# Kernel optimization log

Measured on AMD Instinct MI355X. Metric: run time of the kernel, lower is better.

Reference implementation:

```python
import jax, jax.numpy as jnp
import numpy as np

IN, H, T = 1024, 2048, 2048

def setup_inputs() -> dict:
    key = jax.random.key(0)
    ks = jax.random.split(key, 10)
    x = jax.random.normal(ks[0], (1, T, IN), dtype=jnp.float32)
    # strictly increasing timestamps
    time = jnp.cumsum(jax.random.uniform(ks[1], (T,), dtype=jnp.float32))
    # xavier-ish scaled weights, uniform(0,1) biases as in init_weights
    W_ih = jax.random.normal(ks[2], (4 * H, IN), dtype=jnp.float32) * (1.0 / np.sqrt(IN))
    W_hh = jax.random.normal(ks[3], (4 * H, H), dtype=jnp.float32) * (1.0 / np.sqrt(H))
    b_ih = jax.random.uniform(ks[4], (4 * H,), dtype=jnp.float32)
    b_hh = jax.random.uniform(ks[5], (4 * H,), dtype=jnp.float32)
    decay_w = jax.random.normal(ks[6], (H,), dtype=jnp.float32)
    decay_b = jax.random.uniform(ks[7], (H,), dtype=jnp.float32)
    h0 = jax.random.normal(ks[8], (1, H), dtype=jnp.float32) * 0.1
    c0 = jax.random.normal(ks[9], (1, H), dtype=jnp.float32) * 0.1
    return {"x": x, "time": time, "W_ih": W_ih, "W_hh": W_hh, "b_ih": b_ih,
            "b_hh": b_hh, "decay_w": decay_w, "decay_b": decay_b, "h0": h0, "c0": c0}


def reference(x, time, W_ih, W_hh, b_ih, b_hh, decay_w, decay_b, h0, c0):
    Tn = x.shape[1]
    Hn = h0.shape[1]
    # dt[i] = time[i] - time[i-1], dt[0] = 0
    dt = jnp.concatenate([jnp.zeros((1,), x.dtype), time[1:] - time[:-1]])
    # step i (i>0) decays h with gamma(dt[i-1]); step 0 uses gamma = 1
    dt_prev = jnp.concatenate([jnp.zeros((1,), x.dtype), dt[:-1]])  # [T]
    gamma = jnp.exp(-jax.nn.relu(dt_prev[:, None] * decay_w[None, :] + decay_b[None, :]))  # [T,H]
    gamma = jnp.where((jnp.arange(Tn) > 0)[:, None], gamma, jnp.ones((), x.dtype))
    # precompute input contribution for all steps: [T, 4H]
    xg = x[0] @ W_ih.T + b_ih + b_hh

    def step(carry, inp):
        h, c = carry  # [H], [H]
        xg_t, gamma_t = inp
        h = h * gamma_t
        gates = xg_t + h @ W_hh.T  # [4H]
        i_, f_, g_, o_ = jnp.split(gates, 4)
        i_ = jax.nn.sigmoid(i_)
        f_ = jax.nn.sigmoid(f_)
        g_ = jnp.tanh(g_)
        o_ = jax.nn.sigmoid(o_)
        c = f_ * c + i_ * g_
        h = o_ * jnp.tanh(c)
        return (h, c), h

    (h_f, c_f), hs = jax.lax.scan(step, (h0[0], c0[0]), (xg, gamma))  # hs: [T,H]
    # dot-product attention pooling against final hidden state
    attn = hs @ h_f  # [T]
    w = jax.nn.softmax(attn)
    context = w @ hs  # [H]
    return context[None, :]  # [1, H]
```

## Files before the change

kernel.cpp:

```cpp
#include <hip/hip_runtime.h>
#include <hip/hip_bf16.h>

#define H 2048
#define T 2048
#define INPUT 1024
#define FOURH 8192
#define NBLK 256
#define RING 512

typedef __attribute__((ext_vector_type(8))) short bf16x8;
typedef __attribute__((ext_vector_type(4))) float f32x4_t;

__device__ __forceinline__ short f2bf(float f) {
  union { float f; unsigned u; } v; v.f = f;
  unsigned r = v.u + 0x7FFFu + ((v.u >> 16) & 1u);
  return (short)(r >> 16);
}

__global__ void prep_kernel(const float* __restrict__ x, const float* __restrict__ W_ih,
                            const float* __restrict__ time_, short* __restrict__ xb,
                            short* __restrict__ wb, float* __restrict__ dtp,
                            unsigned* __restrict__ flags) {
  size_t i = (size_t)blockIdx.x * blockDim.x + threadIdx.x;
  size_t stride = (size_t)gridDim.x * blockDim.x;
  if (i < (size_t)T * INPUT) xb[i] = f2bf(x[i]);
  for (size_t j = i; j < (size_t)FOURH * INPUT; j += stride) wb[j] = f2bf(W_ih[j]);
  if (i < T) dtp[i] = (i >= 2) ? (time_[i - 1] - time_[i - 2]) : 0.0f;
  if (i < NBLK) flags[i] = 0u;
}

__global__ void __launch_bounds__(256)
gemm_xg(const short* __restrict__ A, const short* __restrict__ B,
        const float* __restrict__ b_ih, const float* __restrict__ b_hh,
        float* __restrict__ xg) {
  int wave = threadIdx.x >> 6;
  int lane = threadIdx.x & 63;
  int m0 = blockIdx.y << 4;
  int n0 = (blockIdx.x << 6) + (wave << 4);
  int r16 = lane & 15, q = lane >> 4;
  const short* ap = A + (size_t)(m0 + r16) * INPUT + q * 8;
  const short* bp = B + (size_t)(n0 + r16) * INPUT + q * 8;
  f32x4_t acc = {0.f, 0.f, 0.f, 0.f};
#pragma unroll 4
  for (int k = 0; k < INPUT; k += 32) {
    bf16x8 av = *(const bf16x8*)(ap + k);
    bf16x8 bv = *(const bf16x8*)(bp + k);
    acc = __builtin_amdgcn_mfma_f32_16x16x32_bf16(av, bv, acc, 0, 0, 0);
  }
  int n = n0 + r16;
  float bias = b_ih[n] + b_hh[n];
#pragma unroll
  for (int r = 0; r < 4; ++r) {
    int m = m0 + q * 4 + r;
    xg[(size_t)m * FOURH + n] = acc[r] + bias;
  }
}

__device__ __forceinline__ void epoch_bar(unsigned* flags, unsigned e) {
  __syncthreads();
  if (threadIdx.x == 0)
    __hip_atomic_store(&flags[blockIdx.x], e, __ATOMIC_RELEASE, __HIP_MEMORY_SCOPE_AGENT);
  if (threadIdx.x < NBLK) {
    while (__hip_atomic_load(&flags[threadIdx.x], __ATOMIC_RELAXED,
                             __HIP_MEMORY_SCOPE_AGENT) < e) {
    }
  }
  __builtin_amdgcn_fence(__ATOMIC_ACQUIRE, "agent");
  __syncthreads();
}

__global__ void __launch_bounds__(512, 2)
lstm_rec(const float* __restrict__ xg, const float* __restrict__ W_hh,
         const float* __restrict__ decay_w, const float* __restrict__ decay_b,
         const float* __restrict__ h0, const float* __restrict__ c0,
         const float* __restrict__ dtp, float* __restrict__ hs,
         unsigned long long* ring, unsigned* flags) {
  const int wave = threadIdx.x >> 6;
  const int lane = threadIdx.x & 63;
  const int u = (blockIdx.x << 3) + wave;
  __shared__ float lh[H];

  float wreg[4][32];
#pragma unroll
  for (int g = 0; g < 4; ++g) {
    const float* wr = W_hh + (size_t)(g * H + u) * H + lane;
#pragma unroll
    for (int j = 0; j < 32; ++j) wreg[g][j] = wr[(size_t)j << 6];
  }
  const float dw = decay_w[u], db = decay_b[u];
  float c = c0[u];
  if (lane == 0) {
    union { float f; unsigned u; } hv; hv.f = h0[u];
    __hip_atomic_store(&ring[u], (1ull << 32) | hv.u, __ATOMIC_RELAXED,
                       __HIP_MEMORY_SCOPE_AGENT);
  }

  for (int t = 0; t < T; ++t) {
    if ((t & 255) == 0 && t) epoch_bar(flags, (unsigned)(t >> 8));

    float xi = 0.f, xf = 0.f, xgv = 0.f, xo = 0.f, dtn = 0.f;
    if (lane == 0) {
      const float* xr = xg + (size_t)t * FOURH;
      xi = xr[u]; xf = xr[H + u]; xgv = xr[2 * H + u]; xo = xr[3 * H + u];
      if (t + 1 < T) dtn = dtp[t + 1];
    }

    const unsigned want = (unsigned)t + 1u;
    unsigned long long* sp =
        ring + (((size_t)(t & (RING - 1)) << 11) | (unsigned)((wave << 8) + lane));
    unsigned long long w0, w1, w2, w3;
    for (;;) {
      w0 = __hip_atomic_load(sp,       __ATOMIC_RELAXED, __HIP_MEMORY_SCOPE_AGENT);
      w1 = __hip_atomic_load(sp + 64,  __ATOMIC_RELAXED, __HIP_MEMORY_SCOPE_AGENT);
      w2 = __hip_atomic_load(sp + 128, __ATOMIC_RELAXED, __HIP_MEMORY_SCOPE_AGENT);
      w3 = __hip_atomic_load(sp + 192, __ATOMIC_RELAXED, __HIP_MEMORY_SCOPE_AGENT);
      int bad = ((unsigned)(w0 >> 32) != want) | ((unsigned)(w1 >> 32) != want) |
                ((unsigned)(w2 >> 32) != want) | ((unsigned)(w3 >> 32) != want);
      if (!__any(bad)) break;
    }
    {
      float* lw = lh + (wave << 8) + lane;
      union { unsigned u; float f; } v;
      v.u = (unsigned)w0; lw[0]   = v.f;
      v.u = (unsigned)w1; lw[64]  = v.f;
      v.u = (unsigned)w2; lw[128] = v.f;
      v.u = (unsigned)w3; lw[192] = v.f;
    }
    __syncthreads();

    float a0 = 0.f, a1 = 0.f, a2 = 0.f, a3 = 0.f;
#pragma unroll
    for (int j = 0; j < 32; ++j) {
      float h = lh[(j << 6) + lane];
      a0 += wreg[0][j] * h;
      a1 += wreg[1][j] * h;
      a2 += wreg[2][j] * h;
      a3 += wreg[3][j] * h;
    }
#pragma unroll
    for (int s = 32; s >= 1; s >>= 1) {
      a0 += __shfl_xor(a0, s);
      a1 += __shfl_xor(a1, s);
      a2 += __shfl_xor(a2, s);
      a3 += __shfl_xor(a3, s);
    }
    if (lane == 0) {
      float iv = a0 + xi;
      float fv = a1 + xf;
      float gv = a2 + xgv;
      float ov = a3 + xo;
      iv = 1.f / (1.f + __expf(-iv));
      fv = 1.f / (1.f + __expf(-fv));
      gv = tanhf(gv);
      ov = 1.f / (1.f + __expf(-ov));
      c = fv * c + iv * gv;
      float h = ov * tanhf(c);
      hs[(size_t)t * H + u] = h;
      if (t + 1 < T) {
        float gam = __expf(-fmaxf(0.f, dtn * dw + db));
        union { float f; unsigned u; } hv; hv.f = h * gam;
        size_t slot = (size_t)((t + 1) & (RING - 1)) << 11;
        __hip_atomic_store(&ring[slot | (unsigned)u],
                           (((unsigned long long)(t + 2)) << 32) | hv.u,
                           __ATOMIC_RELAXED, __HIP_MEMORY_SCOPE_AGENT);
      }
    }
    __syncthreads();
  }
}

__global__ void attn_k(const float* __restrict__ hs, float* __restrict__ attn) {
  int t = blockIdx.x;
  const float* row = hs + (size_t)t * H;
  const float* hf = hs + (size_t)(T - 1) * H;
  float s = 0.f;
  for (int i = threadIdx.x; i < H; i += 256) s += row[i] * hf[i];
#pragma unroll
  for (int o = 32; o; o >>= 1) s += __shfl_down(s, o);
  __shared__ float wsum[4];
  if ((threadIdx.x & 63) == 0) wsum[threadIdx.x >> 6] = s;
  __syncthreads();
  if (threadIdx.x == 0) attn[t] = wsum[0] + wsum[1] + wsum[2] + wsum[3];
}

__global__ void softmax_k(float* __restrict__ a) {
  int tid = threadIdx.x;
  __shared__ float red[16];
  __shared__ float bcast;
  float m = -1e30f;
  for (int i = tid; i < T; i += 1024) m = fmaxf(m, a[i]);
#pragma unroll
  for (int o = 32; o; o >>= 1) m = fmaxf(m, __shfl_xor(m, o));
  if ((tid & 63) == 0) red[tid >> 6] = m;
  __syncthreads();
  if (tid == 0) {
    float mm = red[0];
    for (int i = 1; i < 16; ++i) mm = fmaxf(mm, red[i]);
    bcast = mm;
  }
  __syncthreads();
  float M = bcast, s = 0.f;
  for (int i = tid; i < T; i += 1024) { float e = __expf(a[i] - M); a[i] = e; s += e; }
#pragma unroll
  for (int o = 32; o; o >>= 1) s += __shfl_xor(s, o);
  if ((tid & 63) == 0) red[tid >> 6] = s;
  __syncthreads();
  if (tid == 0) {
    float ss = 0.f;
    for (int i = 0; i < 16; ++i) ss += red[i];
    bcast = 1.f / ss;
  }
  __syncthreads();
  float inv = bcast;
  for (int i = tid; i < T; i += 1024) a[i] *= inv;
}

__global__ void ctx_k(const float* __restrict__ hs, const float* __restrict__ w,
                      float* __restrict__ out) {
  int h = (blockIdx.x << 8) + threadIdx.x;
  int t0 = blockIdx.y << 6;
  float acc = 0.f;
  for (int t = t0; t < t0 + 64; ++t) acc += w[t] * hs[(size_t)t * H + h];
  atomicAdd(&out[h], acc);
}

extern "C" void kernel_launch(void* const* d_in, const int* in_sizes, int n_in,
                              void* d_out, int out_size, void* d_ws, size_t ws_size,
                              hipStream_t stream) {
  const float* x       = (const float*)d_in[0];
  const float* time_   = (const float*)d_in[1];
  const float* W_ih    = (const float*)d_in[2];
  const float* W_hh    = (const float*)d_in[3];
  const float* b_ih    = (const float*)d_in[4];
  const float* b_hh    = (const float*)d_in[5];
  const float* decay_w = (const float*)d_in[6];
  const float* decay_b = (const float*)d_in[7];
  const float* h0      = (const float*)d_in[8];
  const float* c0      = (const float*)d_in[9];

  char* ws = (char*)d_ws;
  float*    xg   = (float*)ws;
  float*    hs   = (float*)(ws + (64u << 20));
  short*    xb   = (short*)(ws + (80u << 20));
  short*    wb   = (short*)(ws + (84u << 20));
  unsigned long long* ring = (unsigned long long*)(ws + (100u << 20));
  float*    dtp  = (float*)(ws + (108u << 20));
  float*    attn = dtp + T;
  unsigned* flags = (unsigned*)(attn + T);

  prep_kernel<<<8192, 256, 0, stream>>>(x, W_ih, time_, xb, wb, dtp, flags);

  dim3 g1(FOURH / 64, T / 16);
  gemm_xg<<<g1, 256, 0, stream>>>(xb, wb, b_ih, b_hh, xg);

  {
    void* args[] = {&xg, (void*)&W_hh, (void*)&decay_w, (void*)&decay_b,
                    (void*)&h0, (void*)&c0, &dtp, &hs, &ring, &flags};
    (void)hipLaunchCooperativeKernel((void*)lstm_rec, dim3(NBLK), dim3(512), args, 0, stream);
  }

  attn_k<<<T, 256, 0, stream>>>(hs, attn);
  softmax_k<<<1, 1024, 0, stream>>>(attn);
  (void)hipMemsetAsync(d_out, 0, out_size * sizeof(float), stream);
  ctx_k<<<dim3(H / 256, T / 64), 256, 0, stream>>>(hs, attn, (float*)d_out);
}
```

Before: 6.799 ms.

## Vectorize recurrent LDS reads, precompute decay early, reorder GEMM grid

The recurrent kernel now loads W_hh into registers and reads the hidden state from LDS as 16-byte float4 vectors, with each lane owning four contiguous elements. This replaces 32 scalar LDS reads per step with 8 vector reads. The decay factor is computed before the ring spin-wait, off the critical path, and the ring store is issued before the hs store so other blocks see the new state sooner. The xg GEMM switches to a 1D grid that walks M fastest, changing block scheduling order and cache reuse of the weight tiles.

```diff
diff --git a/kernel.cpp b/kernel.cpp
--- a/kernel.cpp
+++ b/kernel.cpp
@@ -11,10 +11,10 @@
 typedef __attribute__((ext_vector_type(8))) short bf16x8;
 typedef __attribute__((ext_vector_type(4))) float f32x4_t;
 
-__device__ __forceinline__ short f2bf(float f) {
+__device__ __forceinline__ unsigned short f2bf(float f) {
   union { float f; unsigned u; } v; v.f = f;
   unsigned r = v.u + 0x7FFFu + ((v.u >> 16) & 1u);
-  return (short)(r >> 16);
+  return (unsigned short)(r >> 16);
 }
 
 __global__ void prep_kernel(const float* __restrict__ x, const float* __restrict__ W_ih,
@@ -23,8 +23,8 @@
                             unsigned* __restrict__ flags) {
   size_t i = (size_t)blockIdx.x * blockDim.x + threadIdx.x;
   size_t stride = (size_t)gridDim.x * blockDim.x;
-  if (i < (size_t)T * INPUT) xb[i] = f2bf(x[i]);
-  for (size_t j = i; j < (size_t)FOURH * INPUT; j += stride) wb[j] = f2bf(W_ih[j]);
+  if (i < (size_t)T * INPUT) xb[i] = (short)f2bf(x[i]);
+  for (size_t j = i; j < (size_t)FOURH * INPUT; j += stride) wb[j] = (short)f2bf(W_ih[j]);
   if (i < T) dtp[i] = (i >= 2) ? (time_[i - 1] - time_[i - 2]) : 0.0f;
   if (i < NBLK) flags[i] = 0u;
 }
@@ -35,8 +35,9 @@
         float* __restrict__ xg) {
   int wave = threadIdx.x >> 6;
   int lane = threadIdx.x & 63;
-  int m0 = blockIdx.y << 4;
-  int n0 = (blockIdx.x << 6) + (wave << 4);
+  int bid = blockIdx.x;
+  int m0 = (bid & 127) << 4;
+  int n0 = ((bid >> 7) << 6) + (wave << 4);
   int r16 = lane & 15, q = lane >> 4;
   const short* ap = A + (size_t)(m0 + r16) * INPUT + q * 8;
   const short* bp = B + (size_t)(n0 + r16) * INPUT + q * 8;
@@ -78,14 +79,15 @@
   const int wave = threadIdx.x >> 6;
   const int lane = threadIdx.x & 63;
   const int u = (blockIdx.x << 3) + wave;
-  __shared__ float lh[H];
+  __shared__ __align__(16) float lh[H];
 
   float wreg[4][32];
 #pragma unroll
   for (int g = 0; g < 4; ++g) {
-    const float* wr = W_hh + (size_t)(g * H + u) * H + lane;
-#pragma unroll
-    for (int j = 0; j < 32; ++j) wreg[g][j] = wr[(size_t)j << 6];
+    const float* wr = W_hh + (size_t)(g * H + u) * H + (lane << 2);
+#pragma unroll
+    for (int p = 0; p < 8; ++p)
+      *(f32x4_t*)&wreg[g][p << 2] = *(const f32x4_t*)(wr + (p << 8));
   }
   const float dw = decay_w[u], db = decay_b[u];
   float c = c0[u];
@@ -98,11 +100,11 @@
   for (int t = 0; t < T; ++t) {
     if ((t & 255) == 0 && t) epoch_bar(flags, (unsigned)(t >> 8));
 
-    float xi = 0.f, xf = 0.f, xgv = 0.f, xo = 0.f, dtn = 0.f;
+    float xi = 0.f, xf = 0.f, xgv = 0.f, xo = 0.f, gam = 0.f;
     if (lane == 0) {
       const float* xr = xg + (size_t)t * FOURH;
       xi = xr[u]; xf = xr[H + u]; xgv = xr[2 * H + u]; xo = xr[3 * H + u];
-      if (t + 1 < T) dtn = dtp[t + 1];
+      if (t + 1 < T) gam = __expf(-fmaxf(0.f, dtp[t + 1] * dw + db));
     }
 
     const unsigned want = (unsigned)t + 1u;
@@ -130,12 +132,16 @@
 
     float a0 = 0.f, a1 = 0.f, a2 = 0.f, a3 = 0.f;
 #pragma unroll
-    for (int j = 0; j < 32; ++j) {
-      float h = lh[(j << 6) + lane];
-      a0 += wreg[0][j] * h;
-      a1 += wreg[1][j] * h;
-      a2 += wreg[2][j] * h;
-      a3 += wreg[3][j] * h;
+    for (int p = 0; p < 8; ++p) {
+      f32x4_t h4 = *(const f32x4_t*)(lh + (p << 8) + (lane << 2));
+#pragma unroll
+      for (int e = 0; e < 4; ++e) {
+        float h = h4[e];
+        a0 += wreg[0][(p << 2) + e] * h;
+        a1 += wreg[1][(p << 2) + e] * h;
+        a2 += wreg[2][(p << 2) + e] * h;
+        a3 += wreg[3][(p << 2) + e] * h;
+      }
     }
 #pragma unroll
     for (int s = 32; s >= 1; s >>= 1) {
@@ -155,15 +161,14 @@
       ov = 1.f / (1.f + __expf(-ov));
       c = fv * c + iv * gv;
       float h = ov * tanhf(c);
-      hs[(size_t)t * H + u] = h;
       if (t + 1 < T) {
-        float gam = __expf(-fmaxf(0.f, dtn * dw + db));
         union { float f; unsigned u; } hv; hv.f = h * gam;
         size_t slot = (size_t)((t + 1) & (RING - 1)) << 11;
         __hip_atomic_store(&ring[slot | (unsigned)u],
                            (((unsigned long long)(t + 2)) << 32) | hv.u,
                            __ATOMIC_RELAXED, __HIP_MEMORY_SCOPE_AGENT);
       }
+      hs[(size_t)t * H + u] = h;
     }
     __syncthreads();
   }
@@ -250,8 +255,7 @@
 
   prep_kernel<<<8192, 256, 0, stream>>>(x, W_ih, time_, xb, wb, dtp, flags);
 
-  dim3 g1(FOURH / 64, T / 16);
-  gemm_xg<<<g1, 256, 0, stream>>>(xb, wb, b_ih, b_hh, xg);
+  gemm_xg<<<16384, 256, 0, stream>>>(xb, wb, b_ih, b_hh, xg);
 
   {
     void* args[] = {&xg, (void*)&W_hh, (void*)&decay_w, (void*)&decay_b,
```

New measurement: 6.437 ms. 5.3% less time.
